# Performance work log

Hardware: AMD Instinct MI355X
Metric: run time of the kernel (lower is better)

## Reference

```python
import jax, jax.numpy as jnp
import numpy as np

NQ, NS, QN, SN = 10000, 500, 4, 10   # num_question, num_skill, q/s neighbor sizes
B, S, D = 32, 200, 128               # batch, seq_len, emb_dim
HOPS = 3


def setup_inputs() -> dict:
    key = jax.random.key(0)
    ks = iter(jax.random.split(key, 40))

    def nrm(shape, scale=0.05):
        return jax.random.normal(next(ks), shape, dtype=jnp.float32) * scale

    return {
        "question": jax.random.randint(next(ks), (B, S), 0, NQ),
        "response": jax.random.randint(next(ks), (B, S), 0, 2),
        "mask": jnp.ones((B, S), dtype=jnp.int32),
        "q_neighbors": jax.random.randint(next(ks), (NQ, QN), 0, NS),  # question -> skill ids
        "s_neighbors": jax.random.randint(next(ks), (NS, SN), 0, NQ),  # skill -> question ids
        "qs_skills": jax.random.randint(next(ks), (NQ, 4), 0, NS),     # related skills per question
        "emb_q": nrm((NQ, D), 1.0),
        "emb_s": nrm((NS, D), 1.0),
        "emb_r": nrm((2, D), 1.0),
        "W_ih": nrm((2 * D, 4 * D)), "b_ih": nrm((4 * D,)), "b_hh": nrm((4 * D,)),
        "ft_W": nrm((D, D)), "ft_b": nrm((D,)),
        "agg_W": nrm((HOPS, D, D)), "agg_b": nrm((HOPS, D)),
        "last_W": nrm((D, D)), "last_b": nrm((D,)),
        "q_W": nrm((D, D)), "q_b": nrm((D,)),
        "k_W": nrm((D, D)), "k_b": nrm((D,)),
        "w_W": nrm((2 * D,)), "w_b": nrm(()),
    }


def reference(question, response, mask, q_neighbors, s_neighbors, qs_skills,
              emb_q, emb_s, emb_r, W_ih, b_ih, b_hh, ft_W, ft_b,
              agg_W, agg_b, last_W, last_b, q_W, q_b, k_W, k_b, w_W, w_b):
    # ---- multi-hop GNN aggregation for every (b, t) question (mask == 1 everywhere) ----
    q_flat = question.reshape(-1)              # [B*S]
    lvl1 = q_neighbors[q_flat]                 # [N, QN]            skill ids
    lvl2 = s_neighbors[lvl1]                   # [N, QN, SN]        question ids
    lvl3 = q_neighbors[lvl2]                   # [N, QN, SN, QN]    skill ids
    embs = [emb_q[q_flat], emb_s[lvl1], emb_q[lvl2], emb_s[lvl3]]
    for i in range(HOPS):
        embs = [jnp.tanh((embs[j] + embs[j + 1].mean(axis=-2)) @ agg_W[j] + agg_b[j])
                for j in range(HOPS - i)]
    agg_emb = jnp.tanh(embs[0] @ last_W + last_b).reshape(B, S, D)

    # ---- per-step input + zero-state LSTMCell (source calls lstm_cell without hx) ----
    q_trans = jax.nn.relu(agg_emb @ ft_W + ft_b)
    x = jnp.concatenate([q_trans, emb_r[response]], axis=-1)   # [B, S, 2D]
    gates = x @ W_ih + b_ih + b_hh                             # h_prev = 0, c_prev = 0
    i_g, f_g, g_g, o_g = jnp.split(gates, 4, axis=-1)
    c = jax.nn.sigmoid(i_g) * jnp.tanh(g_g)
    h = jax.nn.sigmoid(o_g) * jnp.tanh(c)                      # [B, S, D]
    states = h[:, :S - 1]                                      # state written at step t

    # ---- soft-recap attention prediction for q_next = question[:, t+1] ----
    q_next = question[:, 1:]                                   # [B, T], T = S-1
    qs = jnp.concatenate([emb_q[q_next][:, :, None, :], emb_s[qs_skills[q_next]]], axis=2)  # [B,T,5,D]

    inner = jnp.einsum('bnd,btmd->btnm', states, qs)           # state/qs inner products
    a_state = (states @ q_W + q_b) @ w_W[:D]                   # [B, N]  MLP_query on states
    a_qs = (qs @ k_W + k_b) @ w_W[D:]                          # [B, T, 5] MLP_key on qs
    logits = a_state[:, None, :, None] + a_qs[:, :, None, :] + w_b  # [B, T, N, 5]

    t_idx = jnp.arange(S - 1)
    valid = t_idx[None, :] <= t_idx[:, None]                   # [T, N]: states 0..t visible at t
    logits = jnp.where(valid[None, :, :, None], logits, -jnp.inf)
    alpha = jax.nn.softmax(logits.reshape(B, S - 1, -1), axis=-1).reshape(logits.shape)
    pred = jnp.sum(alpha * jax.nn.sigmoid(inner), axis=(2, 3))  # [B, T]

    return jnp.zeros((B, S), jnp.float32).at[:, 1:].set(pred)
```

## Files before the change

### kernel.cpp

```cpp
#include <hip/hip_runtime.h>

typedef unsigned short u16;
typedef unsigned int   u32;

#define NQd 10000
#define NSd 500
#define Bd  32
#define Sd  200
#define Td  199
#define Dd  128
#define NR  6368
#define PB  208

typedef __attribute__((ext_vector_type(8))) short bf16x8;
typedef __attribute__((ext_vector_type(4))) float f32x4;

__device__ __forceinline__ float sigf(float x) {
  return __builtin_amdgcn_rcpf(1.f + __expf(-x));
}
__device__ __forceinline__ float tanh_f(float x) {
  float ax = fminf(fabsf(x), 15.f);
  float e = __expf(2.f * ax);
  float r = 1.f - 2.f * __builtin_amdgcn_rcpf(e + 1.f);
  return copysignf(r, x);
}
__device__ __forceinline__ float bf2f(u16 u) { return __uint_as_float(((u32)u) << 16); }
__device__ __forceinline__ u16 f2bf(float f) {
  u32 b = __float_as_uint(f);
  b += 0x7FFFu + ((b >> 16) & 1u);
  return (u16)(b >> 16);
}
__device__ __forceinline__ void unp2(u32 u, float &a, float &b) {
  a = __uint_as_float(u << 16);
  b = __uint_as_float(u & 0xffff0000u);
}
__device__ __forceinline__ void unpack16(uint4 a0, uint4 a1, float* f) {
  unp2(a0.x, f[0], f[1]);  unp2(a0.y, f[2], f[3]);
  unp2(a0.z, f[4], f[5]);  unp2(a0.w, f[6], f[7]);
  unp2(a1.x, f[8], f[9]);  unp2(a1.y, f[10], f[11]);
  unp2(a1.z, f[12], f[13]); unp2(a1.w, f[14], f[15]);
}

struct Args {
  const int *question, *response, *q_nb, *s_nb, *qs_sk;
  const float *emb_q, *emb_s, *emb_r;
  const float *W_ih, *b_ih, *b_hh, *ft_W, *ft_b, *agg_W, *agg_b, *last_W, *last_b;
  const float *q_W, *q_b, *k_W, *k_b, *w_W;
  u16 *tabA, *tabB, *tabs1, *tabs2, *states, *embq_bf, *embs_bf, *wts, *wiht;
  float *a_state, *qw, *kw, *scal, *er_part, *ev, *invZ, *pred_acc, *pm;
  int *qid_map, *resp_map;
};

struct WF { bf16x8 v[2][4]; };

__device__ __forceinline__ void load_WF(const u16* Wt, int l15, int quad, int cw, WF& w)
{
#pragma unroll
  for (int nt = 0; nt < 2; ++nt)
#pragma unroll
    for (int kc = 0; kc < 4; ++kc)
      w.v[nt][kc] = *(const bf16x8*)&Wt[(long)(cw + nt * 16 + l15) * 128 + kc * 32 + quad * 8];
}

__device__ __forceinline__ void zero_acc(f32x4 acc[2][2]) {
#pragma unroll
  for (int x = 0; x < 2; ++x)
#pragma unroll
    for (int y = 0; y < 2; ++y) acc[x][y] = (f32x4){0.f, 0.f, 0.f, 0.f};
}

__device__ __forceinline__ void mfma_WF(const u16* Al, const WF& w,
                                        int l15, int quad, f32x4 acc[2][2])
{
#pragma unroll
  for (int kc = 0; kc < 4; ++kc) {
    const int ko = kc * 32 + quad * 8;
    bf16x8 a0 = *(const bf16x8*)&Al[l15 * 136 + ko];
    bf16x8 a1 = *(const bf16x8*)&Al[(16 + l15) * 136 + ko];
    acc[0][0] = __builtin_amdgcn_mfma_f32_16x16x32_bf16(a0, w.v[0][kc], acc[0][0], 0, 0, 0);
    acc[0][1] = __builtin_amdgcn_mfma_f32_16x16x32_bf16(a0, w.v[1][kc], acc[0][1], 0, 0, 0);
    acc[1][0] = __builtin_amdgcn_mfma_f32_16x16x32_bf16(a1, w.v[0][kc], acc[1][0], 0, 0, 0);
    acc[1][1] = __builtin_amdgcn_mfma_f32_16x16x32_bf16(a1, w.v[1][kc], acc[1][1], 0, 0, 0);
  }
}

__device__ __forceinline__ void stage_A(const u16* Atab, const u16* Btab,
                                        const int* nbr, int K, int tile0, int rows,
                                        int tid, u16* Al)
{
  int r = tid & 31, k0 = (tid >> 5) * 16;
  int row = tile0 + r; if (row >= rows) row = rows - 1;
  const u16* ap = Atab + (long)row * 128 + k0;
  if (K == 0) {
    *(uint4*)&Al[r * 136 + k0]     = *(const uint4*)ap;
    *(uint4*)&Al[r * 136 + k0 + 8] = *(const uint4*)(ap + 8);
  } else {
    float f[16];
    unpack16(*(const uint4*)ap, *(const uint4*)(ap + 8), f);
    float s[16];
#pragma unroll
    for (int q = 0; q < 16; ++q) s[q] = 0.f;
    for (int l = 0; l < K; ++l) {
      int id = nbr[(long)row * K + l];
      const u16* np = Btab + (long)id * 128 + k0;
      float g[16];
      unpack16(*(const uint4*)np, *(const uint4*)(np + 8), g);
#pragma unroll
      for (int q = 0; q < 16; ++q) s[q] += g[q];
    }
    float inv = 1.f / (float)K;
#pragma unroll
    for (int q = 0; q < 16; ++q) f[q] += s[q] * inv;
    u32 p[8];
#pragma unroll
    for (int q = 0; q < 8; ++q)
      p[q] = (u32)f2bf(f[2 * q]) | ((u32)f2bf(f[2 * q + 1]) << 16);
    *(uint4*)&Al[r * 136 + k0]     = make_uint4(p[0], p[1], p[2], p[3]);
    *(uint4*)&Al[r * 136 + k0 + 8] = make_uint4(p[4], p[5], p[6], p[7]);
  }
}

__device__ __forceinline__ void update_A(const u16* Btab, const int* nbr,
                                         int tile0, int rows, int tid, u16* Al)
{
  int r = tid & 31, k0 = (tid >> 5) * 16;
  int row = tile0 + r; if (row >= rows) row = rows - 1;
  float f[16];
  unpack16(*(const uint4*)&Al[r * 136 + k0], *(const uint4*)&Al[r * 136 + k0 + 8], f);
  float s[16];
#pragma unroll
  for (int q = 0; q < 16; ++q) s[q] = 0.f;
#pragma unroll
  for (int l = 0; l < 4; ++l) {
    int id = nbr[(long)row * 4 + l];
    const u16* np = Btab + (long)id * 128 + k0;
    float g[16];
    unpack16(*(const uint4*)np, *(const uint4*)(np + 8), g);
#pragma unroll
    for (int q = 0; q < 16; ++q) s[q] += g[q];
  }
#pragma unroll
  for (int q = 0; q < 16; ++q) f[q] += s[q] * 0.25f;
  u32 p[8];
#pragma unroll
  for (int q = 0; q < 8; ++q)
    p[q] = (u32)f2bf(f[2 * q]) | ((u32)f2bf(f[2 * q + 1]) << 16);
  *(uint4*)&Al[r * 136 + k0]     = make_uint4(p[0], p[1], p[2], p[3]);
  *(uint4*)&Al[r * 136 + k0 + 8] = make_uint4(p[4], p[5], p[6], p[7]);
}

__device__ __forceinline__ void epi_tanh_global(const f32x4 acc[2][2], const float* cbias,
                                                u16* out, int rows, int tile0,
                                                int l15, int quad, int cw)
{
#pragma unroll
  for (int nt = 0; nt < 2; ++nt) {
    int col = cw + nt * 16 + l15;
    float cb = cbias[col];
#pragma unroll
    for (int mt = 0; mt < 2; ++mt) {
      int rbase = tile0 + mt * 16 + quad * 4;
#pragma unroll
      for (int i = 0; i < 4; ++i) {
        int row = rbase + i;
        if (row >= rows) continue;
        out[(long)row * 128 + col] = f2bf(tanh_f(acc[mt][nt][i] + cb));
      }
    }
  }
}

__device__ __forceinline__ void epi_tanh_lds(const f32x4 acc[2][2], const float* cbias,
                                             u16* Al, int l15, int quad, int cw)
{
#pragma unroll
  for (int nt = 0; nt < 2; ++nt) {
    int col = cw + nt * 16 + l15;
    float cb = cbias[col];
#pragma unroll
    for (int mt = 0; mt < 2; ++mt)
#pragma unroll
      for (int i = 0; i < 4; ++i) {
        int rL = mt * 16 + quad * 4 + i;
        Al[rL * 136 + col] = f2bf(tanh_f(acc[mt][nt][i] + cb));
      }
  }
}

__global__ __launch_bounds__(256) void prep_all(Args a)
{
  const int T = gridDim.x * 256;
  for (int i = blockIdx.x * 256 + threadIdx.x; i < 491106; i += T) {
    if (i < 320000) {
      float4 v = *(const float4*)&a.emb_q[(long)i * 4];
      ((uint2*)a.embq_bf)[i] = make_uint2(
          (u32)f2bf(v.x) | ((u32)f2bf(v.y) << 16),
          (u32)f2bf(v.z) | ((u32)f2bf(v.w) << 16));
    } else if (i < 336000) {
      int c = i - 320000;
      float4 v = *(const float4*)&a.emb_s[(long)c * 4];
      ((uint2*)a.embs_bf)[c] = make_uint2(
          (u32)f2bf(v.x) | ((u32)f2bf(v.y) << 16),
          (u32)f2bf(v.z) | ((u32)f2bf(v.w) << 16));
    } else if (i < 417920) {
      int e = i - 336000;
      int seg = e >> 14, r = e & 16383;
      int col = r >> 7, k = r & 127;
      const float* src = (seg < 3) ? (a.agg_W + seg * 16384)
                                   : (seg == 3 ? a.last_W : a.ft_W);
      a.wts[e] = f2bf(src[k * 128 + col]);
    } else if (i < 483456) {
      int e = i - 417920;
      int col = e >> 7, k = e & 127;
      a.wiht[e] = f2bf(a.W_ih[k * 512 + col]);
    } else if (i < 489824) {
      int j = i - 483456;
      int b = j / Td, s = j - b * Td;
      a.qid_map[j]  = a.question[b * Sd + s];
      a.resp_map[j] = a.response[b * Sd + s];
    } else {
      int s = i - 489824;
      if (s < 128) {
        float acc = 0;
        for (int e = 0; e < 128; ++e) acc += a.q_W[s * 128 + e] * a.w_W[e];
        a.qw[s] = acc;
      } else if (s < 256) {
        int d = s - 128; float acc = 0;
        for (int e = 0; e < 128; ++e) acc += a.k_W[d * 128 + e] * a.w_W[128 + e];
        a.kw[d] = acc;
      } else if (s == 256) {
        float acc = 0;
        for (int e = 0; e < 128; ++e) acc += a.q_b[e] * a.w_W[e];
        a.scal[0] = acc;
      } else if (s == 257) {
        float acc = 0;
        for (int e = 0; e < 128; ++e) acc += a.k_b[e] * a.w_W[128 + e];
        a.scal[1] = acc;
      } else {
        int e2 = s - 258, rr = e2 >> 9, col = e2 & 511;
        float acc = a.b_ih[col] + a.b_hh[col];
        for (int d = 0; d < 128; ++d) acc += a.emb_r[rr * Dd + d] * a.W_ih[(128 + d) * 512 + col];
        a.er_part[rr * 512 + col] = acc;
      }
    }
  }
}

__global__ __launch_bounds__(256) void level1m(Args a)
{
  __shared__ __align__(16) u16 Al[32 * 136];
  const int i = blockIdx.x, tid = threadIdx.x;
  const int lane = tid & 63, wv = tid >> 6;
  const int l15 = lane & 15, quad = lane >> 4, cw = wv * 32;

  if (i >= 329) {
    int item = (i - 329) * 256 + tid;
    if (item >= NR) return;
    int b = item / Td, t = item - b * Td;
    int qn = a.question[b * Sd + t + 1];
    float am[5];
#pragma unroll
    for (int m = 0; m < 5; ++m) {
      const u16* src = (m == 0) ? a.embq_bf + (long)qn * 128
                                : a.embs_bf + (long)a.qs_sk[qn * 4 + (m - 1)] * 128;
      float s = 0.f;
      for (int k = 0; k < 128; k += 8) {
        uint4 u = *(const uint4*)&src[k];
        float f[8];
        unp2(u.x, f[0], f[1]); unp2(u.y, f[2], f[3]);
        unp2(u.z, f[4], f[5]); unp2(u.w, f[6], f[7]);
#pragma unroll
        for (int q = 0; q < 8; ++q) s = fmaf(f[q], a.kw[k + q], s);
      }
      am[m] = s + a.scal[1];
    }
    float mx = am[0];
#pragma unroll
    for (int m = 1; m < 5; ++m) mx = fmaxf(mx, am[m]);
    float ex[5], z = 0.f;
#pragma unroll
    for (int m = 0; m < 5; ++m) { ex[m] = __expf(am[m] - mx); z += ex[m]; }
    float iz = __builtin_amdgcn_rcpf(z);
#pragma unroll
    for (int m = 0; m < 5; ++m) a.pm[((long)b * PB + t) * 5 + m] = ex[m] * iz;
    return;
  }

  f32x4 acc[2][2];
  if (i >= 313) {
    const int tile0 = (i - 313) * 32;
    WF w1; load_WF(a.wts + 16384, l15, quad, cw, w1);
    stage_A(a.embs_bf, a.embq_bf, a.s_nb, 10, tile0, NSd, tid, Al);
    __syncthreads();
    zero_acc(acc);
    mfma_WF(Al, w1, l15, quad, acc);
    epi_tanh_global(acc, a.agg_b + 128, a.tabs1, NSd, tile0, l15, quad, cw);
    return;
  }
  const int tile0 = i * 32;
  WF w2, w0;
  load_WF(a.wts + 2 * 16384, l15, quad, cw, w2);
  load_WF(a.wts, l15, quad, cw, w0);
  stage_A(a.embq_bf, a.embs_bf, a.q_nb, 4, tile0, NQd, tid, Al);
  __syncthreads();
  zero_acc(acc);
  mfma_WF(Al, w2, l15, quad, acc);
  epi_tanh_global(acc, a.agg_b + 256, a.tabA, NQd, tile0, l15, quad, cw);
  zero_acc(acc);
  mfma_WF(Al, w0, l15, quad, acc);
  epi_tanh_global(acc, a.agg_b, a.tabB, NQd, tile0, l15, quad, cw);
}

__global__ __launch_bounds__(256) void g1k(Args a)
{
  __shared__ __align__(16) u16 Al[32 * 136];
  const int tid = threadIdx.x, tile0 = blockIdx.x * 32;
  const int lane = tid & 63, wv = tid >> 6;
  const int l15 = lane & 15, quad = lane >> 4, cw = wv * 32;
  WF w1; load_WF(a.wts + 16384, l15, quad, cw, w1);
  stage_A(a.tabs1, a.tabA, a.s_nb, 10, tile0, NSd, tid, Al);
  __syncthreads();
  f32x4 acc[2][2];
  zero_acc(acc);
  mfma_WF(Al, w1, l15, quad, acc);
  epi_tanh_global(acc, a.agg_b + 128, a.tabs2, NSd, tile0, l15, quad, cw);
}

__global__ __launch_bounds__(256) void chain4(Args a)
{
  __shared__ __align__(16) u16 Al[32 * 136];
  const int tid = threadIdx.x, tile0 = blockIdx.x * 32;
  const int lane = tid & 63, wv = tid >> 6;
  const int l15 = lane & 15, quad = lane >> 4, cw = wv * 32;
  WF w0, w3, w4;
  load_WF(a.wts, l15, quad, cw, w0);
  load_WF(a.wts + 3 * 16384, l15, quad, cw, w3);
  load_WF(a.wts + 4 * 16384, l15, quad, cw, w4);
  f32x4 acc[2][2];

  stage_A(a.tabB, a.tabs1, a.q_nb, 4, tile0, NQd, tid, Al);
  __syncthreads();
  zero_acc(acc);
  mfma_WF(Al, w0, l15, quad, acc);
  __syncthreads();
  epi_tanh_lds(acc, a.agg_b, Al, l15, quad, cw);
  __syncthreads();
  update_A(a.tabs2, a.q_nb, tile0, NQd, tid, Al);
  __syncthreads();
  zero_acc(acc);
  mfma_WF(Al, w0, l15, quad, acc);
  __syncthreads();
  epi_tanh_lds(acc, a.agg_b, Al, l15, quad, cw);
  __syncthreads();
  zero_acc(acc);
  mfma_WF(Al, w3, l15, quad, acc);
  __syncthreads();
  epi_tanh_lds(acc, a.last_b, Al, l15, quad, cw);
  __syncthreads();
  zero_acc(acc);
  mfma_WF(Al, w4, l15, quad, acc);
#pragma unroll
  for (int nt = 0; nt < 2; ++nt) {
    int col = cw + nt * 16 + l15;
    float cb = a.ft_b[col];
#pragma unroll
    for (int mt = 0; mt < 2; ++mt) {
      int rbase = tile0 + mt * 16 + quad * 4;
#pragma unroll
      for (int i = 0; i < 4; ++i) {
        int row = rbase + i;
        if (row >= NQd) continue;
        a.tabA[(long)row * 128 + col] = f2bf(fmaxf(acc[mt][nt][i] + cb, 0.f));
      }
    }
  }
}

__global__ __launch_bounds__(256) void gates_k(Args a)
{
  __shared__ __align__(16) u16 Al[32 * 136];
  __shared__ float hb[32 * 132];
  const int tid = threadIdx.x, tile0 = blockIdx.x * 32;
  const int lane = tid & 63, wv = tid >> 6;
  const int l15 = lane & 15, quad = lane >> 4, cw = wv * 32;
  WF wg0, wg1, wg2;
  load_WF(a.wiht, l15, quad, cw, wg0);
  load_WF(a.wiht + (long)256 * 128, l15, quad, cw, wg1);
  load_WF(a.wiht + (long)384 * 128, l15, quad, cw, wg2);
  {
    int r = tid & 31, k0 = (tid >> 5) * 16;
    int row = tile0 + r;
    int arow = a.qid_map[row];
    const u16* ap = a.tabA + (long)arow * 128 + k0;
    *(uint4*)&Al[r * 136 + k0]     = *(const uint4*)ap;
    *(uint4*)&Al[r * 136 + k0 + 8] = *(const uint4*)(ap + 8);
  }
  __syncthreads();
  f32x4 acc[3][2][2];
  zero_acc(acc[0]); mfma_WF(Al, wg0, l15, quad, acc[0]);
  zero_acc(acc[1]); mfma_WF(Al, wg1, l15, quad, acc[1]);
  zero_acc(acc[2]); mfma_WF(Al, wg2, l15, quad, acc[2]);
#pragma unroll
  for (int nt = 0; nt < 2; ++nt) {
    int colL = cw + nt * 16 + l15;
#pragma unroll
    for (int mt = 0; mt < 2; ++mt) {
#pragma unroll
      for (int i = 0; i < 4; ++i) {
        int rL = mt * 16 + quad * 4 + i;
        int row = tile0 + rL;
        const float* rb = a.er_part + (long)a.resp_map[row] * 512;
        float iv = acc[0][mt][nt][i] + rb[colL];
        float gv = acc[1][mt][nt][i] + rb[256 + colL];
        float ov = acc[2][mt][nt][i] + rb[384 + colL];
        float c = sigf(iv) * tanh_f(gv);
        float h = sigf(ov) * tanh_f(c);
        a.states[(long)row * 128 + colL] = f2bf(h);
        hb[rL * 132 + colL] = h;
      }
    }
  }
  __syncthreads();
#pragma unroll
  for (int rr = 0; rr < 8; ++rr) {
    int rL = wv * 8 + rr;
    float p = hb[rL * 132 + lane] * a.qw[lane] + hb[rL * 132 + 64 + lane] * a.qw[64 + lane];
#pragma unroll
    for (int off = 32; off > 0; off >>= 1) p += __shfl_xor(p, off);
    if (lane == 0) a.a_state[tile0 + rL] = p + a.scal[0];
  }
}

__global__ __launch_bounds__(256) void bprep(Args a)
{
  __shared__ float red[256];
  __shared__ float evl[256];
  const int b = blockIdx.x, tid = threadIdx.x;
  float v = (tid < Td) ? a.a_state[b * Td + tid] : -1e30f;
  red[tid] = v; __syncthreads();
  for (int s = 128; s > 0; s >>= 1) { if (tid < s) red[tid] = fmaxf(red[tid], red[tid + s]); __syncthreads(); }
  float gmax = red[0];
  float e = (tid < Td) ? __expf(v - gmax) : 0.f;
  evl[tid] = e;
  if (tid < Td) { a.ev[b * PB + tid] = e; a.pred_acc[b * PB + tid] = 0.f; }
  __syncthreads();
  for (int off = 1; off < 256; off <<= 1) {
    float add = (tid >= off) ? evl[tid - off] : 0.f;
    __syncthreads();
    evl[tid] += add;
    __syncthreads();
  }
  if (tid < Td) a.invZ[b * PB + tid] = 1.f / evl[tid];
}

__global__ __launch_bounds__(256) void gk_pred(Args a)
{
  const int n0 = blockIdx.x * 32;
  const int c0 = blockIdx.y * 128;
  const int b  = blockIdx.z;
  int c_hi = c0 + 127; if (c_hi > 994) c_hi = 994;
  const int tmax = c_hi / 5, tmin = c0 / 5;
  if (n0 > tmax) return;

  __shared__ __align__(16) u16 smem[21760];
  __shared__ float predl[32];
  u16* Ql = smem;
  u16* Sl = smem + 17408;
  const int tid = threadIdx.x;
  if (tid < 32) predl[tid] = 0.f;
  {
    int r = tid & 31, k0 = (tid >> 5) * 16;
    int n = n0 + r; if (n > 198) n = 198;
    const u16* sp = a.states + ((long)b * Td + n) * 128 + k0;
    *(uint4*)&Sl[r * 136 + k0]     = *(const uint4*)sp;
    *(uint4*)&Sl[r * 136 + k0 + 8] = *(const uint4*)(sp + 8);
  }
  {
    int j = tid >> 1, k0 = (tid & 1) * 64;
    int col = c0 + j;
    uint4* dst = (uint4*)&Ql[j * 136 + k0];
    if (col < 995) {
      int t = col / 5, m = col - t * 5;
      int qn = a.question[b * Sd + t + 1];
      const u16* src = (m == 0) ? a.embq_bf + (long)qn * 128
                                : a.embs_bf + (long)a.qs_sk[qn * 4 + (m - 1)] * 128;
      src += k0;
#pragma unroll
      for (int q = 0; q < 8; ++q) dst[q] = ((const uint4*)src)[q];
    } else {
      uint4 z = make_uint4(0, 0, 0, 0);
#pragma unroll
      for (int q = 0; q < 8; ++q) dst[q] = z;
    }
  }
  __syncthreads();
  const int lane = tid & 63, wv = tid >> 6;
  const int l15 = lane & 15, quad = lane >> 4, cw = wv * 32;
  f32x4 acc[2][2];
  zero_acc(acc);
#pragma unroll
  for (int kc = 0; kc < 4; ++kc) {
    const int ko = kc * 32 + quad * 8;
    bf16x8 af[2], bfv[2];
    af[0]  = *(const bf16x8*)&Sl[l15 * 136 + ko];
    af[1]  = *(const bf16x8*)&Sl[(16 + l15) * 136 + ko];
    bfv[0] = *(const bf16x8*)&Ql[(cw + l15) * 136 + ko];
    bfv[1] = *(const bf16x8*)&Ql[(cw + 16 + l15) * 136 + ko];
#pragma unroll
    for (int mt = 0; mt < 2; ++mt)
#pragma unroll
      for (int nt = 0; nt < 2; ++nt)
        acc[mt][nt] = __builtin_amdgcn_mfma_f32_16x16x32_bf16(af[mt], bfv[nt], acc[mt][nt], 0, 0, 0);
  }

#pragma unroll
  for (int nt = 0; nt < 2; ++nt) {
    int col = c0 + cw + nt * 16 + l15;
    if (col >= 995) continue;
    int t = col / 5, m = col - t * 5;
    float pmv = a.pm[((long)b * PB + t) * 5 + m];
    float part = 0.f;
#pragma unroll
    for (int mt = 0; mt < 2; ++mt) {
      int nb = n0 + mt * 16 + quad * 4;
      if (nb > t) continue;
      float4 ev4 = *(const float4*)&a.ev[b * PB + nb];
      float evv[4] = {ev4.x, ev4.y, ev4.z, ev4.w};
#pragma unroll
      for (int i = 0; i < 4; ++i) {
        int n = nb + i;
        if (n > t || n > 198) continue;
        part += evv[i] * sigf(acc[mt][nt][i]);
      }
    }
    part *= pmv;
    if (part != 0.f) atomicAdd(&predl[t - tmin], part);
  }
  __syncthreads();
  const int tcnt = tmax - tmin + 1;
  if (tid < tcnt) {
    float pv = predl[tid];
    if (pv != 0.f) atomicAdd(&a.pred_acc[b * PB + tmin + tid], pv);
  }
}

__global__ __launch_bounds__(256) void finalize(Args a, float* __restrict__ out)
{
  int i = blockIdx.x * 256 + threadIdx.x;
  if (i >= Bd * Sd) return;
  int b = i / Sd, s = i - b * Sd;
  out[i] = (s == 0) ? 0.f : a.pred_acc[b * PB + s - 1] * a.invZ[b * PB + s - 1];
}

extern "C" void kernel_launch(void* const* d_in, const int* in_sizes, int n_in,
                              void* d_out, int out_size, void* d_ws, size_t ws_size,
                              hipStream_t stream)
{
  Args a;
  a.question = (const int*)d_in[0];
  a.response = (const int*)d_in[1];
  a.q_nb     = (const int*)d_in[3];
  a.s_nb     = (const int*)d_in[4];
  a.qs_sk    = (const int*)d_in[5];
  a.emb_q    = (const float*)d_in[6];
  a.emb_s    = (const float*)d_in[7];
  a.emb_r    = (const float*)d_in[8];
  a.W_ih     = (const float*)d_in[9];
  a.b_ih     = (const float*)d_in[10];
  a.b_hh     = (const float*)d_in[11];
  a.ft_W     = (const float*)d_in[12];
  a.ft_b     = (const float*)d_in[13];
  a.agg_W    = (const float*)d_in[14];
  a.agg_b    = (const float*)d_in[15];
  a.last_W   = (const float*)d_in[16];
  a.last_b   = (const float*)d_in[17];
  a.q_W      = (const float*)d_in[18];
  a.q_b      = (const float*)d_in[19];
  a.k_W      = (const float*)d_in[20];
  a.k_b      = (const float*)d_in[21];
  a.w_W      = (const float*)d_in[22];

  u16* wsu = (u16*)d_ws;
  const long NT = 1280000, ST = 64000, RT = (long)NR * Dd;
  a.tabA  = wsu;
  a.tabB  = a.tabA + NT;
  a.tabs1 = a.tabB + NT;
  a.tabs2 = a.tabs1 + ST;
  a.states  = a.tabs2 + ST;
  a.embq_bf = a.states + RT;
  a.embs_bf = a.embq_bf + NT;
  a.wts     = a.embs_bf + ST;
  a.wiht    = a.wts + 5 * 16384;
  float* fp = (float*)(a.wiht + 65536);
  a.a_state = fp;
  a.qw      = fp + 6368;
  a.kw      = fp + 6496;
  a.scal    = fp + 6624;
  a.er_part = fp + 6640;
  a.ev       = fp + 7664;
  a.invZ     = a.ev + 32 * PB;
  a.pred_acc = a.invZ + 32 * PB;
  a.pm       = a.pred_acc + 32 * PB;
  a.qid_map  = (int*)(a.pm + 32 * PB * 5);
  a.resp_map = a.qid_map + NR;

  float* out = (float*)d_out;

  prep_all<<<640, 256, 0, stream>>>(a);
  level1m<<<354, 256, 0, stream>>>(a);
  g1k<<<16, 256, 0, stream>>>(a);
  chain4<<<313, 256, 0, stream>>>(a);
  gates_k<<<199, 256, 0, stream>>>(a);
  bprep<<<Bd, 256, 0, stream>>>(a);
  gk_pred<<<dim3(7, 8, Bd), 256, 0, stream>>>(a);
  finalize<<<25, 256, 0, stream>>>(a, out);
}
```

Baseline: 196.6 us.

## Compact chain4 to unique referenced questions and fuse finalize into gk_pred

Builds a deduplicated list of question ids that appear in the batch, using an atomic flag, counter and index map inside prep_all. chain4 then runs only over those unique rows instead of all 10000 questions, and gates_k remaps through newidx. The finalize kernel and the pred_acc buffer are removed: prep_all zeroes the output and gk_pred atomically adds scaled contributions straight into it. This adds a memset, atomic contention in prep_all, and an order-dependent compaction in exchange for far less GEMM work in chain4.

Result: faster. 191.0 us (-2.8%).

```diff
diff --git a/kernel.cpp b/kernel.cpp
--- a/kernel.cpp
+++ b/kernel.cpp
@@ -47,8 +47,8 @@
   const float *W_ih, *b_ih, *b_hh, *ft_W, *ft_b, *agg_W, *agg_b, *last_W, *last_b;
   const float *q_W, *q_b, *k_W, *k_b, *w_W;
   u16 *tabA, *tabB, *tabs1, *tabs2, *states, *embq_bf, *embs_bf, *wts, *wiht;
-  float *a_state, *qw, *kw, *scal, *er_part, *ev, *invZ, *pred_acc, *pm;
-  int *qid_map, *resp_map;
+  float *a_state, *qw, *kw, *scal, *er_part, *ev, *invZ, *pm;
+  int *qid_map, *resp_map, *flag, *cnt, *list, *newidx;
 };
 
 struct WF { bf16x8 v[2][4]; };
@@ -85,12 +85,13 @@
 }
 
 __device__ __forceinline__ void stage_A(const u16* Atab, const u16* Btab,
-                                        const int* nbr, int K, int tile0, int rows,
-                                        int tid, u16* Al)
+                                        const int* nbr, int K, const int* rowmap,
+                                        int tile0, int rows, int tid, u16* Al)
 {
   int r = tid & 31, k0 = (tid >> 5) * 16;
   int row = tile0 + r; if (row >= rows) row = rows - 1;
-  const u16* ap = Atab + (long)row * 128 + k0;
+  int arow = rowmap ? rowmap[row] : row;
+  const u16* ap = Atab + (long)arow * 128 + k0;
   if (K == 0) {
     *(uint4*)&Al[r * 136 + k0]     = *(const uint4*)ap;
     *(uint4*)&Al[r * 136 + k0 + 8] = *(const uint4*)(ap + 8);
@@ -101,7 +102,7 @@
 #pragma unroll
     for (int q = 0; q < 16; ++q) s[q] = 0.f;
     for (int l = 0; l < K; ++l) {
-      int id = nbr[(long)row * K + l];
+      int id = nbr[(long)arow * K + l];
       const u16* np = Btab + (long)id * 128 + k0;
       float g[16];
       unpack16(*(const uint4*)np, *(const uint4*)(np + 8), g);
@@ -121,10 +122,12 @@
 }
 
 __device__ __forceinline__ void update_A(const u16* Btab, const int* nbr,
-                                         int tile0, int rows, int tid, u16* Al)
+                                         const int* rowmap, int tile0, int rows,
+                                         int tid, u16* Al)
 {
   int r = tid & 31, k0 = (tid >> 5) * 16;
   int row = tile0 + r; if (row >= rows) row = rows - 1;
+  int arow = rowmap ? rowmap[row] : row;
   float f[16];
   unpack16(*(const uint4*)&Al[r * 136 + k0], *(const uint4*)&Al[r * 136 + k0 + 8], f);
   float s[16];
@@ -132,7 +135,7 @@
   for (int q = 0; q < 16; ++q) s[q] = 0.f;
 #pragma unroll
   for (int l = 0; l < 4; ++l) {
-    int id = nbr[(long)row * 4 + l];
+    int id = nbr[(long)arow * 4 + l];
     const u16* np = Btab + (long)id * 128 + k0;
     float g[16];
     unpack16(*(const uint4*)np, *(const uint4*)(np + 8), g);
@@ -187,10 +190,10 @@
   }
 }
 
-__global__ __launch_bounds__(256) void prep_all(Args a)
+__global__ __launch_bounds__(256) void prep_all(Args a, float* __restrict__ out)
 {
   const int T = gridDim.x * 256;
-  for (int i = blockIdx.x * 256 + threadIdx.x; i < 491106; i += T) {
+  for (int i = blockIdx.x * 256 + threadIdx.x; i < 497506; i += T) {
     if (i < 320000) {
       float4 v = *(const float4*)&a.emb_q[(long)i * 4];
       ((uint2*)a.embq_bf)[i] = make_uint2(
@@ -216,9 +219,15 @@
     } else if (i < 489824) {
       int j = i - 483456;
       int b = j / Td, s = j - b * Td;
-      a.qid_map[j]  = a.question[b * Sd + s];
+      int qid = a.question[b * Sd + s];
+      a.qid_map[j]  = qid;
       a.resp_map[j] = a.response[b * Sd + s];
-    } else {
+      if (atomicExch(&a.flag[qid], 1) == 0) {
+        int idx = atomicAdd(a.cnt, 1);
+        a.list[idx] = qid;
+        a.newidx[qid] = idx;
+      }
+    } else if (i < 491106) {
       int s = i - 489824;
       if (s < 128) {
         float acc = 0;
@@ -242,6 +251,8 @@
         for (int d = 0; d < 128; ++d) acc += a.emb_r[rr * Dd + d] * a.W_ih[(128 + d) * 512 + col];
         a.er_part[rr * 512 + col] = acc;
       }
+    } else {
+      out[i - 491106] = 0.f;
     }
   }
 }
@@ -290,7 +301,7 @@
   if (i >= 313) {
     const int tile0 = (i - 313) * 32;
     WF w1; load_WF(a.wts + 16384, l15, quad, cw, w1);
-    stage_A(a.embs_bf, a.embq_bf, a.s_nb, 10, tile0, NSd, tid, Al);
+    stage_A(a.embs_bf, a.embq_bf, a.s_nb, 10, nullptr, tile0, NSd, tid, Al);
     __syncthreads();
     zero_acc(acc);
     mfma_WF(Al, w1, l15, quad, acc);
@@ -301,7 +312,7 @@
   WF w2, w0;
   load_WF(a.wts + 2 * 16384, l15, quad, cw, w2);
   load_WF(a.wts, l15, quad, cw, w0);
-  stage_A(a.embq_bf, a.embs_bf, a.q_nb, 4, tile0, NQd, tid, Al);
+  stage_A(a.embq_bf, a.embs_bf, a.q_nb, 4, nullptr, tile0, NQd, tid, Al);
   __syncthreads();
   zero_acc(acc);
   mfma_WF(Al, w2, l15, quad, acc);
@@ -318,7 +329,7 @@
   const int lane = tid & 63, wv = tid >> 6;
   const int l15 = lane & 15, quad = lane >> 4, cw = wv * 32;
   WF w1; load_WF(a.wts + 16384, l15, quad, cw, w1);
-  stage_A(a.tabs1, a.tabA, a.s_nb, 10, tile0, NSd, tid, Al);
+  stage_A(a.tabs1, a.tabA, a.s_nb, 10, nullptr, tile0, NSd, tid, Al);
   __syncthreads();
   f32x4 acc[2][2];
   zero_acc(acc);
@@ -328,8 +339,11 @@
 
 __global__ __launch_bounds__(256) void chain4(Args a)
 {
+  const int cnt = *a.cnt;
+  const int tile0 = blockIdx.x * 32;
+  if (tile0 >= cnt) return;
   __shared__ __align__(16) u16 Al[32 * 136];
-  const int tid = threadIdx.x, tile0 = blockIdx.x * 32;
+  const int tid = threadIdx.x;
   const int lane = tid & 63, wv = tid >> 6;
   const int l15 = lane & 15, quad = lane >> 4, cw = wv * 32;
   WF w0, w3, w4;
@@ -338,14 +352,14 @@
   load_WF(a.wts + 4 * 16384, l15, quad, cw, w4);
   f32x4 acc[2][2];
 
-  stage_A(a.tabB, a.tabs1, a.q_nb, 4, tile0, NQd, tid, Al);
+  stage_A(a.tabB, a.tabs1, a.q_nb, 4, a.list, tile0, cnt, tid, Al);
   __syncthreads();
   zero_acc(acc);
   mfma_WF(Al, w0, l15, quad, acc);
   __syncthreads();
   epi_tanh_lds(acc, a.agg_b, Al, l15, quad, cw);
   __syncthreads();
-  update_A(a.tabs2, a.q_nb, tile0, NQd, tid, Al);
+  update_A(a.tabs2, a.q_nb, a.list, tile0, cnt, tid, Al);
   __syncthreads();
   zero_acc(acc);
   mfma_WF(Al, w0, l15, quad, acc);
@@ -369,7 +383,7 @@
 #pragma unroll
       for (int i = 0; i < 4; ++i) {
         int row = rbase + i;
-        if (row >= NQd) continue;
+        if (row >= cnt) continue;
         a.tabA[(long)row * 128 + col] = f2bf(fmaxf(acc[mt][nt][i] + cb, 0.f));
       }
     }
@@ -390,7 +404,7 @@
   {
     int r = tid & 31, k0 = (tid >> 5) * 16;
     int row = tile0 + r;
-    int arow = a.qid_map[row];
+    int arow = a.newidx[a.qid_map[row]];
     const u16* ap = a.tabA + (long)arow * 128 + k0;
     *(uint4*)&Al[r * 136 + k0]     = *(const uint4*)ap;
     *(uint4*)&Al[r * 136 + k0 + 8] = *(const uint4*)(ap + 8);
@@ -442,7 +456,7 @@
   float gmax = red[0];
   float e = (tid < Td) ? __expf(v - gmax) : 0.f;
   evl[tid] = e;
-  if (tid < Td) { a.ev[b * PB + tid] = e; a.pred_acc[b * PB + tid] = 0.f; }
+  if (tid < Td) a.ev[b * PB + tid] = e;
   __syncthreads();
   for (int off = 1; off < 256; off <<= 1) {
     float add = (tid >= off) ? evl[tid - off] : 0.f;
@@ -453,7 +467,7 @@
   if (tid < Td) a.invZ[b * PB + tid] = 1.f / evl[tid];
 }
 
-__global__ __launch_bounds__(256) void gk_pred(Args a)
+__global__ __launch_bounds__(256) void gk_pred(Args a, float* __restrict__ out)
 {
   const int n0 = blockIdx.x * 32;
   const int c0 = blockIdx.y * 128;
@@ -539,17 +553,11 @@
   __syncthreads();
   const int tcnt = tmax - tmin + 1;
   if (tid < tcnt) {
+    int t = tmin + tid;
     float pv = predl[tid];
-    if (pv != 0.f) atomicAdd(&a.pred_acc[b * PB + tmin + tid], pv);
-  }
-}
-
-__global__ __launch_bounds__(256) void finalize(Args a, float* __restrict__ out)
-{
-  int i = blockIdx.x * 256 + threadIdx.x;
-  if (i >= Bd * Sd) return;
-  int b = i / Sd, s = i - b * Sd;
-  out[i] = (s == 0) ? 0.f : a.pred_acc[b * PB + s - 1] * a.invZ[b * PB + s - 1];
+    if (pv != 0.f)
+      atomicAdd(&out[b * Sd + t + 1], pv * a.invZ[b * PB + t]);
+  }
 }
 
 extern "C" void kernel_launch(void* const* d_in, const int* in_sizes, int n_in,
@@ -597,21 +605,24 @@
   a.kw      = fp + 6496;
   a.scal    = fp + 6624;
   a.er_part = fp + 6640;
-  a.ev       = fp + 7664;
-  a.invZ     = a.ev + 32 * PB;
-  a.pred_acc = a.invZ + 32 * PB;
-  a.pm       = a.pred_acc + 32 * PB;
+  a.ev      = fp + 7664;
+  a.invZ    = a.ev + 32 * PB;
+  a.pm      = a.invZ + 32 * PB;
   a.qid_map  = (int*)(a.pm + 32 * PB * 5);
   a.resp_map = a.qid_map + NR;
+  a.flag     = a.resp_map + NR;
+  a.cnt      = a.flag + NQd;
+  a.list     = a.cnt + 4;
+  a.newidx   = a.list + NQd;
 
   float* out = (float*)d_out;
 
-  prep_all<<<640, 256, 0, stream>>>(a);
+  hipMemsetAsync(a.flag, 0, (NQd + 4) * sizeof(int), stream);
+  prep_all<<<640, 256, 0, stream>>>(a, out);
   level1m<<<354, 256, 0, stream>>>(a);
   g1k<<<16, 256, 0, stream>>>(a);
-  chain4<<<313, 256, 0, stream>>>(a);
+  chain4<<<199, 256, 0, stream>>>(a);
   gates_k<<<199, 256, 0, stream>>>(a);
   bprep<<<Bd, 256, 0, stream>>>(a);
-  gk_pred<<<dim3(7, 8, Bd), 256, 0, stream>>>(a);
-  finalize<<<25, 256, 0, stream>>>(a, out);
-}
+  gk_pred<<<dim3(7, 8, Bd), 256, 0, stream>>>(a, out);
+}
```
